# Kernel optimization log

Hardware: AMD Instinct MI355X
Metric: run time of the kernel (lower is better)

## Reference

```python
import jax, jax.numpy as jnp
import numpy as np

B, T, CIN, H, W = 8, 16, 16, 64, 64
HID, K = 64, 3


def _conv(x, w, b):
    # x: [B, C, H, W], w: [O, C, K, K] -> [B, O, H, W], 'same' padding
    y = jax.lax.conv_general_dilated(x, w, window_strides=(1, 1), padding='SAME',
                                     dimension_numbers=('NCHW', 'OIHW', 'NCHW'))
    return y + b[None, :, None, None]


def setup_inputs() -> dict:
    key = jax.random.key(0)
    ks = jax.random.split(key, 9)
    cin_h = CIN + HID
    s_conv = 1.0 / np.sqrt(cin_h * K * K)
    s_lin = 1.0 / np.sqrt(cin_h)
    return {
        'x': jax.random.normal(ks[0], (B, T, CIN, H, W), dtype=jnp.float32),
        'Wf': jax.random.uniform(ks[1], (HID, cin_h, K, K), jnp.float32, -s_conv, s_conv),
        'bf': jax.random.uniform(ks[2], (HID,), jnp.float32, -s_conv, s_conv),
        'Wi': jax.random.uniform(ks[3], (HID, cin_h, K, K), jnp.float32, -s_conv, s_conv),
        'bi': jax.random.uniform(ks[4], (HID,), jnp.float32, -s_conv, s_conv),
        'Wc': jax.random.uniform(ks[5], (HID, cin_h, K, K), jnp.float32, -s_conv, s_conv),
        'bc': jax.random.uniform(ks[6], (HID,), jnp.float32, -s_conv, s_conv),
        'Wo': jax.random.uniform(ks[7], (HID, cin_h), jnp.float32, -s_lin, s_lin),
        'bo': jax.random.uniform(ks[8], (HID,), jnp.float32, -s_lin, s_lin),
    }


def reference(x, Wf, bf, Wi, bi, Wc, bc, Wo, bo):
    # x: [B, T, CIN, H, W]
    b, t, cin, h, w = x.shape
    h0 = jnp.zeros((b, HID, h, w), x.dtype)
    c0 = jnp.zeros((b, HID, h, w), x.dtype)

    def step(carry, xt):
        hs, cs = carry
        xc = jnp.concatenate([xt, hs], axis=1)          # [B, CIN+HID, H, W]
        f = jax.nn.sigmoid(_conv(xc, Wf, bf))
        i = jax.nn.sigmoid(_conv(xc, Wi, bi))
        g = jnp.tanh(_conv(xc, Wc, bc))
        # Linear over channel dim (torch applies it on transpose(1,3))
        o = jax.nn.sigmoid(jnp.einsum('bchw,oc->bohw', xc, Wo) + bo[None, :, None, None])
        cs = cs * f + i * g
        hs = jnp.tanh(cs) * o
        return (hs, cs), None

    xs = jnp.swapaxes(x, 0, 1)                          # time-major [T, B, CIN, H, W]
    (hT, cT), _ = jax.lax.scan(step, (h0, c0), xs)
    return hT, cT
```

## Files before the change

### kernel.cpp

```cpp
#include <hip/hip_runtime.h>


#define B_ 8
#define T_ 16
#define CIN_ 16
#define HID_ 64
#define H_ 64
#define W_ 64
#define HW_ (H_*W_)
#define CTOT_ 80
#define XS_ROW 66
#define XS_CH 104
#define XS_SIZE (4*XS_ROW*XS_CH)
#define CSTRIDE_ (B_*HID_*HW_)

typedef __attribute__((ext_vector_type(8))) short short8;
typedef __attribute__((ext_vector_type(4))) float f32x4;

__device__ __forceinline__ unsigned short f2bf(float f){
    unsigned u = __float_as_uint(f);
    u = (u + 0x7FFFu + ((u >> 16) & 1u)) >> 16;
    return (unsigned short)u;
}
__device__ __forceinline__ float sigm_(float v){ return 1.0f/(1.0f + __expf(-v)); }
__device__ __forceinline__ float tanh_(float v){ return 2.0f/(1.0f + __expf(-2.0f*v)) - 1.0f; }

__global__ void prep_wfrag(const float* __restrict__ Wf, const float* __restrict__ Wi,
                           const float* __restrict__ Wc, const float* __restrict__ Wo,
                           const float* __restrict__ bf, const float* __restrict__ bi,
                           const float* __restrict__ bc, const float* __restrict__ bo,
                           unsigned short* __restrict__ Wfrag){
    int idx = blockIdx.x*256 + threadIdx.x;
    int j    = idx & 7;
    int lane = (idx >> 3) & 63;
    int frag = idx >> 9;
    int ng = frag & 15;
    int tc = frag >> 4;
    int cc = tc % 3, tap = tc / 3;
    int n = ng*16 + (lane & 15);
    int g = n >> 6, o = n & 63;
    int c = cc*32 + ((lane >> 4) << 3) + j;
    int ky = tap / 3, kx = tap % 3;
    float v = 0.0f;
    if (c < CTOT_){
        if (g == 0)      v = Wf[((o*CTOT_ + c)*3 + ky)*3 + kx];
        else if (g == 1) v = Wi[((o*CTOT_ + c)*3 + ky)*3 + kx];
        else if (g == 2) v = Wc[((o*CTOT_ + c)*3 + ky)*3 + kx];
        else             v = (tap == 4) ? Wo[o*CTOT_ + c] : 0.0f;
    } else if (c == CTOT_ && tap == 4){
        v = (g==0) ? bf[o] : (g==1) ? bi[o] : (g==2) ? bc[o] : bo[o];
    }
    Wfrag[idx] = f2bf(v);
}

__global__ void prep_xbf(const float* __restrict__ x, unsigned short* __restrict__ xbf){
    int idx = blockIdx.x*256 + threadIdx.x;
    int px = idx & 63;
    int y  = (idx >> 6) & 63;
    int bt = idx >> 12;
    const float* src = x + (size_t)bt*CIN_*HW_ + y*W_ + px;
    unsigned short tmp[16];
    #pragma unroll
    for (int c = 0; c < 16; ++c) tmp[c] = f2bf(src[(size_t)c*HW_]);
    uint4* dst = (uint4*)(xbf + (size_t)idx*16);
    dst[0] = *(uint4*)(tmp);
    dst[1] = *(uint4*)(tmp + 8);
}

__global__ __launch_bounds__(512, 2) void lstm_step(
    const unsigned short* __restrict__ xbf,
    const unsigned short* __restrict__ Wfrag,
    float* __restrict__ cbuf,
    const unsigned short* __restrict__ hin,
    unsigned short* __restrict__ hout,
    float* __restrict__ out,
    int t)
{
    __shared__ __align__(16) unsigned short Xs[XS_SIZE];
    const int id   = blockIdx.x;
    const int xcd  = id & 7;
    const int j    = id >> 3;
    const int b    = j >> 2;
    const int y0   = xcd*8 + ((j & 3) << 1);
    const int tid  = threadIdx.x;
    const int lane = tid & 63;
    const int wid  = tid >> 6;
    const int wm   = wid >> 2;
    const int wn   = wid & 3;
    const int l15  = lane & 15;
    const int q    = lane >> 4;

    uint4 z4; z4.x=z4.y=z4.z=z4.w=0u;
    for (int i = tid; i < XS_SIZE/8; i += 512) ((uint4*)Xs)[i] = z4;
    __syncthreads();

    {
        int row = tid >> 7, rem = tid & 127;
        int px = rem >> 1, ch8 = rem & 1;
        int yy = y0 + row - 1;
        if (yy >= 0 && yy < H_){
            uint4 v = *(const uint4*)(xbf + ((((size_t)(b*T_ + t)*H_ + yy)*W_ + px)*16 + ch8*8));
            *(uint4*)(Xs + ((size_t)(row*XS_ROW + px + 1))*XS_CH + ch8*8) = v;
        }
    }
    if (t > 0){
        #pragma unroll
        for (int k = 0; k < 4; ++k){
            int i = tid + (k << 9);
            int row = i >> 9, rem = i & 511;
            int px = rem >> 3, ch8 = rem & 7;
            int yy = y0 + row - 1;
            if (yy >= 0 && yy < H_){
                uint4 v = *(const uint4*)(hin + ((((size_t)b*H_ + yy)*W_ + px)*HID_ + ch8*8));
                *(uint4*)(Xs + (size_t)(row*XS_ROW + px + 1)*XS_CH + CIN_ + ch8*8) = v;
            }
        }
    }
    for (int i = tid; i < 4*XS_ROW; i += 512)
        Xs[i*XS_CH + CTOT_] = 0x3F80;
    __syncthreads();

    f32x4 acc[4][4];
    #pragma unroll
    for (int g = 0; g < 4; ++g){
        #pragma unroll
        for (int mf = 0; mf < 4; ++mf) acc[g][mf] = (f32x4)0.0f;
    }

    short8 aC[4], bC[3], bO;
    {
        const unsigned short* ap = Xs + (size_t)(wm*XS_ROW + l15)*XS_CH + q*8;
        #pragma unroll
        for (int mf = 0; mf < 4; ++mf) aC[mf] = *(const short8*)(ap + mf*16*XS_CH);
        const unsigned short* bp = Wfrag + (size_t)wn*512 + lane*8;
        #pragma unroll
        for (int g = 0; g < 3; ++g) bC[g] = *(const short8*)(bp + ((size_t)g << 11));
    }
    for (int cc = 0; cc < 3; ++cc){
        #pragma unroll 1
        for (int tap = 0; tap < 9; ++tap){
            int ncc = cc, ntap = tap + 1;
            if (ntap == 9){ ntap = 0; ++ncc; }
            const bool have = (ncc < 3);
            short8 aN[4], bN[3];
            if (have){
                const int nky = ntap/3, nkx = ntap - 3*(ntap/3);
                const unsigned short* ap =
                    Xs + (size_t)((wm + nky)*XS_ROW + l15 + nkx)*XS_CH + ncc*32 + q*8;
                #pragma unroll
                for (int mf = 0; mf < 4; ++mf) aN[mf] = *(const short8*)(ap + mf*16*XS_CH);
                const unsigned short* bp =
                    Wfrag + ((size_t)((ntap*3 + ncc)*16 + wn) << 9) + lane*8;
                #pragma unroll
                for (int g = 0; g < 3; ++g) bN[g] = *(const short8*)(bp + ((size_t)g << 11));
            }
            if (tap == 3)
                bO = *(const short8*)(Wfrag + ((size_t)((4*3 + cc)*16 + 12 + wn) << 9) + lane*8);
            if (tap == 4){
                #pragma unroll
                for (int mf = 0; mf < 4; ++mf)
                    acc[3][mf] = __builtin_amdgcn_mfma_f32_16x16x32_bf16(aC[mf], bO, acc[3][mf], 0,0,0);
            }
            #pragma unroll
            for (int g = 0; g < 3; ++g){
                #pragma unroll
                for (int mf = 0; mf < 4; ++mf)
                    acc[g][mf] = __builtin_amdgcn_mfma_f32_16x16x32_bf16(aC[mf], bC[g], acc[g][mf], 0,0,0);
            }
            if (have){
                #pragma unroll
                for (int mf = 0; mf < 4; ++mf) aC[mf] = aN[mf];
                bC[0]=bN[0]; bC[1]=bN[1]; bC[2]=bN[2];
            }
        }
    }

    const int o = wn*16 + l15;
    const int y = y0 + wm;
    #pragma unroll
    for (int mf = 0; mf < 4; ++mf){
        #pragma unroll
        for (int r = 0; r < 4; ++r){
            const int px = mf*16 + q*4 + r;
            const float fv = sigm_(acc[0][mf][r]);
            const float iv = sigm_(acc[1][mf][r]);
            const float gv = tanh_(acc[2][mf][r]);
            const float ov = sigm_(acc[3][mf][r]);
            const size_t cidx = (((size_t)(b*H_ + y)*W_ + px)*HID_ + o);
            const float cprev = t ? cbuf[cidx] : 0.0f;
            const float cn = cprev*fv + iv*gv;
            const float hn = tanh_(cn)*ov;
            if (t < T_-1){
                cbuf[cidx] = cn;
                hout[cidx] = f2bf(hn);
            } else {
                const size_t oidx = ((((size_t)(b*HID_ + o))*H_ + y)*W_ + px);
                out[oidx] = hn;
                out[CSTRIDE_ + oidx] = cn;
            }
        }
    }
}

extern "C" void kernel_launch(void* const* d_in, const int* in_sizes, int n_in,
                              void* d_out, int out_size, void* d_ws, size_t ws_size,
                              hipStream_t stream){
    const float* x  = (const float*)d_in[0];
    const float* Wf = (const float*)d_in[1];
    const float* bf = (const float*)d_in[2];
    const float* Wi = (const float*)d_in[3];
    const float* bi = (const float*)d_in[4];
    const float* Wc = (const float*)d_in[5];
    const float* bc = (const float*)d_in[6];
    const float* Wo = (const float*)d_in[7];
    const float* bo = (const float*)d_in[8];

    unsigned short* Wfrag = (unsigned short*)d_ws;
    unsigned short* xbf   = (unsigned short*)((char*)d_ws + 442368);
    float*          cbuf  = (float*)((char*)d_ws + 442368 + 16777216);
    unsigned short* hbfA  = (unsigned short*)((char*)d_ws + 442368 + 16777216 + 8388608);
    unsigned short* hbfB  = hbfA + CSTRIDE_;

    prep_wfrag<<<dim3(864), dim3(256), 0, stream>>>(Wf, Wi, Wc, Wo, bf, bi, bc, bo, Wfrag);
    prep_xbf<<<dim3(2048), dim3(256), 0, stream>>>(x, xbf);

    for (int t = 0; t < T_; ++t){
        const unsigned short* hi = (t & 1) ? hbfA : hbfB;
        unsigned short*       ho = (t & 1) ? hbfB : hbfA;
        lstm_step<<<dim3(256), dim3(512), 0, stream>>>(
            xbf, Wfrag, cbuf, hi, ho, (float*)d_out, t);
    }
}
```

Measured before the change: 420.4 us.

## Double block threads to 1024 with half-row warp tiles and early global loads

Each block now runs 16 waves instead of 8. Every wave computes half a 64-pixel row (two M fragments instead of four), which doubles the waves available per block to hide MFMA and LDS latency and cuts per-wave accumulator registers. The global loads of x and h are issued into registers before the LDS zero-fill barrier, so their latency overlaps the clear. The cost is more B-fragment (weight) loads per block, since each wave re-reads the weights for fewer pixels. The launch bounds also ask for 4 blocks per CU, which may force register spilling.

```diff
diff --git a/kernel.cpp b/kernel.cpp
--- a/kernel.cpp
+++ b/kernel.cpp
@@ -67,7 +67,7 @@
     dst[1] = *(uint4*)(tmp + 8);
 }
 
-__global__ __launch_bounds__(512, 2) void lstm_step(
+__global__ __launch_bounds__(1024, 4) void lstm_step(
     const unsigned short* __restrict__ xbf,
     const unsigned short* __restrict__ Wfrag,
     float* __restrict__ cbuf,
@@ -85,53 +85,65 @@
     const int tid  = threadIdx.x;
     const int lane = tid & 63;
     const int wid  = tid >> 6;
+    const int wn   = wid & 3;
     const int wm   = wid >> 2;
-    const int wn   = wid & 3;
+    const int wrow = wm >> 1;
+    const int wx0  = (wm & 1) << 5;
     const int l15  = lane & 15;
     const int q    = lane >> 4;
 
+    uint4 xv; bool xok = false;
+    int xrow = 0, xpx = 0, xch8 = 0;
+    if (tid < 512){
+        xrow = tid >> 7; int rem = tid & 127; xpx = rem >> 1; xch8 = rem & 1;
+        int yy = y0 + xrow - 1;
+        if (yy >= 0 && yy < H_){
+            xok = true;
+            xv = *(const uint4*)(xbf + ((((size_t)(b*T_ + t)*H_ + yy)*W_ + xpx)*16 + xch8*8));
+        }
+    }
+    uint4 hv[2]; bool hok[2] = {false, false};
+    int hrow[2], hpx[2], hch8[2];
+    if (t > 0){
+        #pragma unroll
+        for (int k = 0; k < 2; ++k){
+            int i = tid + (k << 10);
+            hrow[k] = i >> 9; int rem = i & 511; hpx[k] = rem >> 3; hch8[k] = rem & 7;
+            int yy = y0 + hrow[k] - 1;
+            if (yy >= 0 && yy < H_){
+                hok[k] = true;
+                hv[k] = *(const uint4*)(hin + ((((size_t)b*H_ + yy)*W_ + hpx[k])*HID_ + hch8[k]*8));
+            }
+        }
+    }
+
     uint4 z4; z4.x=z4.y=z4.z=z4.w=0u;
-    for (int i = tid; i < XS_SIZE/8; i += 512) ((uint4*)Xs)[i] = z4;
+    for (int i = tid; i < XS_SIZE/8; i += 1024) ((uint4*)Xs)[i] = z4;
     __syncthreads();
 
-    {
-        int row = tid >> 7, rem = tid & 127;
-        int px = rem >> 1, ch8 = rem & 1;
-        int yy = y0 + row - 1;
-        if (yy >= 0 && yy < H_){
-            uint4 v = *(const uint4*)(xbf + ((((size_t)(b*T_ + t)*H_ + yy)*W_ + px)*16 + ch8*8));
-            *(uint4*)(Xs + ((size_t)(row*XS_ROW + px + 1))*XS_CH + ch8*8) = v;
-        }
-    }
+    if (xok)
+        *(uint4*)(Xs + ((size_t)(xrow*XS_ROW + xpx + 1))*XS_CH + xch8*8) = xv;
     if (t > 0){
         #pragma unroll
-        for (int k = 0; k < 4; ++k){
-            int i = tid + (k << 9);
-            int row = i >> 9, rem = i & 511;
-            int px = rem >> 3, ch8 = rem & 7;
-            int yy = y0 + row - 1;
-            if (yy >= 0 && yy < H_){
-                uint4 v = *(const uint4*)(hin + ((((size_t)b*H_ + yy)*W_ + px)*HID_ + ch8*8));
-                *(uint4*)(Xs + (size_t)(row*XS_ROW + px + 1)*XS_CH + CIN_ + ch8*8) = v;
-            }
-        }
-    }
-    for (int i = tid; i < 4*XS_ROW; i += 512)
-        Xs[i*XS_CH + CTOT_] = 0x3F80;
+        for (int k = 0; k < 2; ++k)
+            if (hok[k])
+                *(uint4*)(Xs + (size_t)(hrow[k]*XS_ROW + hpx[k] + 1)*XS_CH + CIN_ + hch8[k]*8) = hv[k];
+    }
+    if (tid < 4*XS_ROW)
+        Xs[tid*XS_CH + CTOT_] = 0x3F80;
     __syncthreads();
 
-    f32x4 acc[4][4];
+    f32x4 acc[4][2];
     #pragma unroll
     for (int g = 0; g < 4; ++g){
-        #pragma unroll
-        for (int mf = 0; mf < 4; ++mf) acc[g][mf] = (f32x4)0.0f;
-    }
-
-    short8 aC[4], bC[3], bO;
+        acc[g][0] = (f32x4)0.0f; acc[g][1] = (f32x4)0.0f;
+    }
+
+    short8 aC[2], bC[3], bO;
     {
-        const unsigned short* ap = Xs + (size_t)(wm*XS_ROW + l15)*XS_CH + q*8;
-        #pragma unroll
-        for (int mf = 0; mf < 4; ++mf) aC[mf] = *(const short8*)(ap + mf*16*XS_CH);
+        const unsigned short* ap = Xs + (size_t)(wrow*XS_ROW + wx0 + l15)*XS_CH + q*8;
+        aC[0] = *(const short8*)(ap);
+        aC[1] = *(const short8*)(ap + 16*XS_CH);
         const unsigned short* bp = Wfrag + (size_t)wn*512 + lane*8;
         #pragma unroll
         for (int g = 0; g < 3; ++g) bC[g] = *(const short8*)(bp + ((size_t)g << 11));
@@ -142,13 +154,13 @@
             int ncc = cc, ntap = tap + 1;
             if (ntap == 9){ ntap = 0; ++ncc; }
             const bool have = (ncc < 3);
-            short8 aN[4], bN[3];
+            short8 aN[2], bN[3];
             if (have){
                 const int nky = ntap/3, nkx = ntap - 3*(ntap/3);
                 const unsigned short* ap =
-                    Xs + (size_t)((wm + nky)*XS_ROW + l15 + nkx)*XS_CH + ncc*32 + q*8;
-                #pragma unroll
-                for (int mf = 0; mf < 4; ++mf) aN[mf] = *(const short8*)(ap + mf*16*XS_CH);
+                    Xs + (size_t)((wrow + nky)*XS_ROW + wx0 + l15 + nkx)*XS_CH + ncc*32 + q*8;
+                aN[0] = *(const short8*)(ap);
+                aN[1] = *(const short8*)(ap + 16*XS_CH);
                 const unsigned short* bp =
                     Wfrag + ((size_t)((ntap*3 + ncc)*16 + wn) << 9) + lane*8;
                 #pragma unroll
@@ -157,31 +169,28 @@
             if (tap == 3)
                 bO = *(const short8*)(Wfrag + ((size_t)((4*3 + cc)*16 + 12 + wn) << 9) + lane*8);
             if (tap == 4){
-                #pragma unroll
-                for (int mf = 0; mf < 4; ++mf)
-                    acc[3][mf] = __builtin_amdgcn_mfma_f32_16x16x32_bf16(aC[mf], bO, acc[3][mf], 0,0,0);
+                acc[3][0] = __builtin_amdgcn_mfma_f32_16x16x32_bf16(aC[0], bO, acc[3][0], 0,0,0);
+                acc[3][1] = __builtin_amdgcn_mfma_f32_16x16x32_bf16(aC[1], bO, acc[3][1], 0,0,0);
             }
             #pragma unroll
             for (int g = 0; g < 3; ++g){
-                #pragma unroll
-                for (int mf = 0; mf < 4; ++mf)
-                    acc[g][mf] = __builtin_amdgcn_mfma_f32_16x16x32_bf16(aC[mf], bC[g], acc[g][mf], 0,0,0);
+                acc[g][0] = __builtin_amdgcn_mfma_f32_16x16x32_bf16(aC[0], bC[g], acc[g][0], 0,0,0);
+                acc[g][1] = __builtin_amdgcn_mfma_f32_16x16x32_bf16(aC[1], bC[g], acc[g][1], 0,0,0);
             }
             if (have){
-                #pragma unroll
-                for (int mf = 0; mf < 4; ++mf) aC[mf] = aN[mf];
+                aC[0]=aN[0]; aC[1]=aN[1];
                 bC[0]=bN[0]; bC[1]=bN[1]; bC[2]=bN[2];
             }
         }
     }
 
     const int o = wn*16 + l15;
-    const int y = y0 + wm;
+    const int y = y0 + wrow;
     #pragma unroll
-    for (int mf = 0; mf < 4; ++mf){
+    for (int mf = 0; mf < 2; ++mf){
         #pragma unroll
         for (int r = 0; r < 4; ++r){
-            const int px = mf*16 + q*4 + r;
+            const int px = wx0 + mf*16 + q*4 + r;
             const float fv = sigm_(acc[0][mf][r]);
             const float iv = sigm_(acc[1][mf][r]);
             const float gv = tanh_(acc[2][mf][r]);
@@ -227,7 +236,7 @@
     for (int t = 0; t < T_; ++t){
         const unsigned short* hi = (t & 1) ? hbfA : hbfB;
         unsigned short*       ho = (t & 1) ? hbfB : hbfA;
-        lstm_step<<<dim3(256), dim3(512), 0, stream>>>(
+        lstm_step<<<dim3(256), dim3(1024), 0, stream>>>(
             xbf, Wfrag, cbuf, hi, ho, (float*)d_out, t);
     }
 }
```

Result: slower. 472.9 us (+12.5%).

## Split LSTM step into one-row blocks and prefetch inputs into registers

Applied to the files above, without the earlier changes.

Each block now handles one output row with 4 waves instead of two rows with 8 waves, and the launch doubles the grid to 512 blocks of 256 threads, which shrinks shared memory to a 3-row halo. Global loads of x, h and the previous cell state are issued into registers before shared memory is written. Only the halo and padding regions are zeroed instead of the whole tile. The aim is to hide global-load latency and raise occupancy, at the cost of more halo rows re-read per output row and dead leftover code.

```diff
diff --git a/kernel.cpp b/kernel.cpp
--- a/kernel.cpp
+++ b/kernel.cpp
@@ -11,7 +11,7 @@
 #define CTOT_ 80
 #define XS_ROW 66
 #define XS_CH 104
-#define XS_SIZE (4*XS_ROW*XS_CH)
+#define XS_SIZE (3*XS_ROW*XS_CH)
 #define CSTRIDE_ (B_*HID_*HW_)
 
 typedef __attribute__((ext_vector_type(8))) short short8;
@@ -67,7 +67,7 @@
     dst[1] = *(uint4*)(tmp + 8);
 }
 
-__global__ __launch_bounds__(512, 2) void lstm_step(
+__global__ __launch_bounds__(256, 2) void lstm_step(
     const unsigned short* __restrict__ xbf,
     const unsigned short* __restrict__ Wfrag,
     float* __restrict__ cbuf,
@@ -80,44 +80,107 @@
     const int id   = blockIdx.x;
     const int xcd  = id & 7;
     const int j    = id >> 3;
-    const int b    = j >> 2;
-    const int y0   = xcd*8 + ((j & 3) << 1);
+    const int y    = xcd*8 + (j & 7);
+    const int b    = j >> 3;
     const int tid  = threadIdx.x;
     const int lane = tid & 63;
-    const int wid  = tid >> 6;
-    const int wm   = wid >> 2;
-    const int wn   = wid & 3;
+    const int wn   = tid >> 6;
     const int l15  = lane & 15;
     const int q    = lane >> 4;
 
+    uint4 xv[2]; bool xok[2] = {false,false};
+    int xrow[2], xpx[2], xch8[2];
+    #pragma unroll
+    for (int k = 0; k < 2; ++k){
+        int i = tid + (k << 8);
+        if (i < 384){
+            xrow[k] = i >> 7; int rem = i & 127; xpx[k] = rem >> 1; xch8[k] = rem & 1;
+            int yy = y + xrow[k] - 1;
+            if (yy >= 0 && yy < H_){
+                xok[k] = true;
+                xv[k] = *(const uint4*)(xbf + ((((size_t)(b*T_ + t)*H_ + yy)*W_ + xpx[k])*16 + xch8[k]*8));
+            }
+        }
+    }
+    uint4 hv[6]; bool hok[6] = {false,false,false,false,false,false};
+    int hrow[6], hpx[6], hch8[6];
+    if (t > 0){
+        #pragma unroll
+        for (int k = 0; k < 6; ++k){
+            int i = tid + (k << 8);
+            hrow[k] = i >> 9; int rem = i & 511; hpx[k] = rem >> 3; hch8[k] = rem & 7;
+            int yy = y + hrow[k] - 1;
+            if (yy >= 0 && yy < H_){
+                hok[k] = true;
+                hv[k] = *(const uint4*)(hin + ((((size_t)b*H_ + yy)*W_ + hpx[k])*HID_ + hch8[k]*8));
+            }
+        }
+    }
+    const int o = wn*16 + l15;
+    float cpv[8];
+    if (t > 0){
+        #pragma unroll
+        for (int mf = 0; mf < 2; ++mf)
+            #pragma unroll
+            for (int r = 0; r < 4; ++r){
+                const int pxo = (mf*2+ (q>>1))*16 + 0;
+                (void)pxo;
+            }
+        #pragma unroll
+        for (int u = 0; u < 8; ++u){
+            const int mf = u >> 2, r = u & 3;
+            const int pxo = mf*16 + q*4 + r;
+            (void)pxo;
+        }
+    }
+    float cp[4][4];
+    if (t > 0){
+        #pragma unroll
+        for (int mf = 0; mf < 4; ++mf)
+            #pragma unroll
+            for (int r = 0; r < 4; ++r){
+                const int pxo = mf*16 + q*4 + r;
+                cp[mf][r] = cbuf[(((size_t)(b*H_ + y)*W_ + pxo)*HID_ + o)];
+            }
+    }
+
     uint4 z4; z4.x=z4.y=z4.z=z4.w=0u;
-    for (int i = tid; i < XS_SIZE/8; i += 512) ((uint4*)Xs)[i] = z4;
-    __syncthreads();
-
-    {
-        int row = tid >> 7, rem = tid & 127;
-        int px = rem >> 1, ch8 = rem & 1;
-        int yy = y0 + row - 1;
-        if (yy >= 0 && yy < H_){
-            uint4 v = *(const uint4*)(xbf + ((((size_t)(b*T_ + t)*H_ + yy)*W_ + px)*16 + ch8*8));
-            *(uint4*)(Xs + ((size_t)(row*XS_ROW + px + 1))*XS_CH + ch8*8) = v;
-        }
-    }
-    if (t > 0){
-        #pragma unroll
-        for (int k = 0; k < 4; ++k){
-            int i = tid + (k << 9);
-            int row = i >> 9, rem = i & 511;
-            int px = rem >> 3, ch8 = rem & 7;
-            int yy = y0 + row - 1;
-            if (yy >= 0 && yy < H_){
-                uint4 v = *(const uint4*)(hin + ((((size_t)b*H_ + yy)*W_ + px)*HID_ + ch8*8));
-                *(uint4*)(Xs + (size_t)(row*XS_ROW + px + 1)*XS_CH + CIN_ + ch8*8) = v;
-            }
-        }
-    }
-    for (int i = tid; i < 4*XS_ROW; i += 512)
-        Xs[i*XS_CH + CTOT_] = 0x3F80;
+    if (tid < 3*XS_ROW){
+        unsigned short* p = Xs + (size_t)tid*XS_CH;
+        *(uint4*)(p + 80) = z4;
+        *(uint4*)(p + 88) = z4;
+        p[CTOT_] = 0x3F80;
+    }
+    if (tid < 60){
+        int pp = tid/10, chunk = tid - pp*10;
+        int row = pp >> 1, px = (pp & 1) ? 65 : 0;
+        *(uint4*)(Xs + (size_t)(row*XS_ROW + px)*XS_CH + chunk*8) = z4;
+    }
+    if (y == 0 || y == H_-1){
+        int row = (y == 0) ? 0 : 2;
+        for (int i = tid; i < 640; i += 256){
+            int px = 1 + i/10, chunk = i - (i/10)*10;
+            *(uint4*)(Xs + (size_t)(row*XS_ROW + px)*XS_CH + chunk*8) = z4;
+        }
+    }
+    if (t == 0){
+        for (int i = tid; i < 1536; i += 256){
+            int row = i >> 9; int rem = i & 511;
+            int px = 1 + (rem >> 3), chunk = rem & 7;
+            *(uint4*)(Xs + (size_t)(row*XS_ROW + px)*XS_CH + CIN_ + chunk*8) = z4;
+        }
+    }
+
+    #pragma unroll
+    for (int k = 0; k < 2; ++k)
+        if (xok[k])
+            *(uint4*)(Xs + (size_t)(xrow[k]*XS_ROW + xpx[k] + 1)*XS_CH + xch8[k]*8) = xv[k];
+    if (t > 0){
+        #pragma unroll
+        for (int k = 0; k < 6; ++k)
+            if (hok[k])
+                *(uint4*)(Xs + (size_t)(hrow[k]*XS_ROW + hpx[k] + 1)*XS_CH + CIN_ + hch8[k]*8) = hv[k];
+    }
     __syncthreads();
 
     f32x4 acc[4][4];
@@ -129,7 +192,7 @@
 
     short8 aC[4], bC[3], bO;
     {
-        const unsigned short* ap = Xs + (size_t)(wm*XS_ROW + l15)*XS_CH + q*8;
+        const unsigned short* ap = Xs + (size_t)l15*XS_CH + q*8;
         #pragma unroll
         for (int mf = 0; mf < 4; ++mf) aC[mf] = *(const short8*)(ap + mf*16*XS_CH);
         const unsigned short* bp = Wfrag + (size_t)wn*512 + lane*8;
@@ -146,7 +209,7 @@
             if (have){
                 const int nky = ntap/3, nkx = ntap - 3*(ntap/3);
                 const unsigned short* ap =
-                    Xs + (size_t)((wm + nky)*XS_ROW + l15 + nkx)*XS_CH + ncc*32 + q*8;
+                    Xs + (size_t)(nky*XS_ROW + l15 + nkx)*XS_CH + ncc*32 + q*8;
                 #pragma unroll
                 for (int mf = 0; mf < 4; ++mf) aN[mf] = *(const short8*)(ap + mf*16*XS_CH);
                 const unsigned short* bp =
@@ -175,8 +238,6 @@
         }
     }
 
-    const int o = wn*16 + l15;
-    const int y = y0 + wm;
     #pragma unroll
     for (int mf = 0; mf < 4; ++mf){
         #pragma unroll
@@ -187,7 +248,7 @@
             const float gv = tanh_(acc[2][mf][r]);
             const float ov = sigm_(acc[3][mf][r]);
             const size_t cidx = (((size_t)(b*H_ + y)*W_ + px)*HID_ + o);
-            const float cprev = t ? cbuf[cidx] : 0.0f;
+            const float cprev = t ? cp[mf][r] : 0.0f;
             const float cn = cprev*fv + iv*gv;
             const float hn = tanh_(cn)*ov;
             if (t < T_-1){
@@ -227,7 +288,7 @@
     for (int t = 0; t < T_; ++t){
         const unsigned short* hi = (t & 1) ? hbfA : hbfB;
         unsigned short*       ho = (t & 1) ? hbfB : hbfA;
-        lstm_step<<<dim3(256), dim3(512), 0, stream>>>(
+        lstm_step<<<dim3(512), dim3(256), 0, stream>>>(
             xbf, Wfrag, cbuf, hi, ho, (float*)d_out, t);
     }
 }
```

After: 663.8 us. +57.9%, slower.

## Issue global loads before LDS zeroing, zero only halo regions, unroll tap loop

Applied to the files above, without the earlier changes.

Global loads of the x and h tiles are now issued into registers first, so their latency overlaps the LDS initialisation, and the full shared-memory zero fill plus its barrier is dropped. Only the halo columns, padding channels, edge rows and (at t=0) the hidden region are zeroed. The tap loop is unrolled by 3 and the Wo fragment load is moved earlier to hide its latency. This costs extra registers and more complex boundary logic, and missing a region in the zeroing would give wrong results.

```diff
diff --git a/kernel.cpp b/kernel.cpp
--- a/kernel.cpp
+++ b/kernel.cpp
@@ -90,34 +90,68 @@
     const int l15  = lane & 15;
     const int q    = lane >> 4;
 
-    uint4 z4; z4.x=z4.y=z4.z=z4.w=0u;
-    for (int i = tid; i < XS_SIZE/8; i += 512) ((uint4*)Xs)[i] = z4;
-    __syncthreads();
-
+    uint4 xv; bool xok = false;
+    int xrow = tid >> 7, xpx, xch8;
     {
-        int row = tid >> 7, rem = tid & 127;
-        int px = rem >> 1, ch8 = rem & 1;
-        int yy = y0 + row - 1;
+        int rem = tid & 127; xpx = rem >> 1; xch8 = rem & 1;
+        int yy = y0 + xrow - 1;
         if (yy >= 0 && yy < H_){
-            uint4 v = *(const uint4*)(xbf + ((((size_t)(b*T_ + t)*H_ + yy)*W_ + px)*16 + ch8*8));
-            *(uint4*)(Xs + ((size_t)(row*XS_ROW + px + 1))*XS_CH + ch8*8) = v;
-        }
-    }
+            xok = true;
+            xv = *(const uint4*)(xbf + ((((size_t)(b*T_ + t)*H_ + yy)*W_ + xpx)*16 + xch8*8));
+        }
+    }
+    uint4 hv[4]; bool hok[4] = {false,false,false,false};
+    int hrow[4], hpx[4], hch8[4];
     if (t > 0){
         #pragma unroll
         for (int k = 0; k < 4; ++k){
             int i = tid + (k << 9);
-            int row = i >> 9, rem = i & 511;
-            int px = rem >> 3, ch8 = rem & 7;
-            int yy = y0 + row - 1;
+            hrow[k] = i >> 9; int rem = i & 511; hpx[k] = rem >> 3; hch8[k] = rem & 7;
+            int yy = y0 + hrow[k] - 1;
             if (yy >= 0 && yy < H_){
-                uint4 v = *(const uint4*)(hin + ((((size_t)b*H_ + yy)*W_ + px)*HID_ + ch8*8));
-                *(uint4*)(Xs + (size_t)(row*XS_ROW + px + 1)*XS_CH + CIN_ + ch8*8) = v;
-            }
-        }
-    }
-    for (int i = tid; i < 4*XS_ROW; i += 512)
-        Xs[i*XS_CH + CTOT_] = 0x3F80;
+                hok[k] = true;
+                hv[k] = *(const uint4*)(hin + ((((size_t)b*H_ + yy)*W_ + hpx[k])*HID_ + hch8[k]*8));
+            }
+        }
+    }
+
+    uint4 z4; z4.x=z4.y=z4.z=z4.w=0u;
+    if (tid < 4*XS_ROW){
+        unsigned short* p = Xs + (size_t)tid*XS_CH;
+        *(uint4*)(p + 80) = z4;
+        *(uint4*)(p + 88) = z4;
+        p[CTOT_] = 0x3F80;
+    }
+    if (tid < 80){
+        int pp = tid/10, chunk = tid - pp*10;
+        int row = pp >> 1, px = (pp & 1) ? 65 : 0;
+        *(uint4*)(Xs + (size_t)(row*XS_ROW + px)*XS_CH + chunk*8) = z4;
+    }
+    if (y0 == 0 || y0 == H_-2){
+        int row = (y0 == 0) ? 0 : 3;
+        for (int i = tid; i < 640; i += 512){
+            int px = 1 + i/10, chunk = i - (i/10)*10;
+            *(uint4*)(Xs + (size_t)(row*XS_ROW + px)*XS_CH + chunk*8) = z4;
+        }
+    }
+    if (t == 0){
+        #pragma unroll
+        for (int k = 0; k < 4; ++k){
+            int i = tid + (k << 9);
+            int row = i >> 9; int rem = i & 511;
+            int px = 1 + (rem >> 3), chunk = rem & 7;
+            *(uint4*)(Xs + (size_t)(row*XS_ROW + px)*XS_CH + CIN_ + chunk*8) = z4;
+        }
+    }
+
+    if (xok)
+        *(uint4*)(Xs + (size_t)(xrow*XS_ROW + xpx + 1)*XS_CH + xch8*8) = xv;
+    if (t > 0){
+        #pragma unroll
+        for (int k = 0; k < 4; ++k)
+            if (hok[k])
+                *(uint4*)(Xs + (size_t)(hrow[k]*XS_ROW + hpx[k] + 1)*XS_CH + CIN_ + hch8[k]*8) = hv[k];
+    }
     __syncthreads();
 
     f32x4 acc[4][4];
@@ -137,7 +171,7 @@
         for (int g = 0; g < 3; ++g) bC[g] = *(const short8*)(bp + ((size_t)g << 11));
     }
     for (int cc = 0; cc < 3; ++cc){
-        #pragma unroll 1
+        #pragma unroll 3
         for (int tap = 0; tap < 9; ++tap){
             int ncc = cc, ntap = tap + 1;
             if (ntap == 9){ ntap = 0; ++ncc; }
@@ -154,7 +188,7 @@
                 #pragma unroll
                 for (int g = 0; g < 3; ++g) bN[g] = *(const short8*)(bp + ((size_t)g << 11));
             }
-            if (tap == 3)
+            if (tap == 1)
                 bO = *(const short8*)(Wfrag + ((size_t)((4*3 + cc)*16 + 12 + wn) << 9) + lane*8);
             if (tap == 4){
                 #pragma unroll
```

New measurement: 440.3 us. 4.7% more time.
